# Performance work log

Measured on AMD Instinct MI355X. Metric: run time of the kernel, lower is better.

## Reference

```python
import jax, jax.numpy as jnp
import numpy as np


def _psf2otf(psf, shape):
    """Pad psf to `shape`, circularly shift so kernel center is at (0,0), FFT2."""
    pad = np.zeros(shape, dtype=np.float64)
    pad[: psf.shape[0], : psf.shape[1]] = psf
    for ax, k in enumerate(psf.shape):
        pad = np.roll(pad, -(k // 2), axis=ax)
    return np.fft.fft2(pad)


def setup_inputs() -> dict:
    key = jax.random.key(0)
    B, C, H, W = 32, 3, 512, 512
    output = jax.random.normal(key, (B, C, H, W), dtype=jnp.float32)
    return {"output": output}


def reference(output) -> jnp.ndarray:
    B, C, H, W = output.shape
    # Frequency-domain gradient filters (static, computed at trace time).
    fx = jnp.asarray(_psf2otf(np.array([[-1.0, 1.0]]), (H, W)), dtype=jnp.complex64)
    fy = jnp.asarray(_psf2otf(np.array([[-1.0], [1.0]]), (H, W)), dtype=jnp.complex64)
    # One batched FFT over (B, C, H, W) instead of B*C separate fft2 calls.
    F = jnp.fft.fft2(output)            # (B, C, H, W) complex64
    gx = jnp.fft.ifft2(F * fx)          # horizontal gradient (complex)
    gy = jnp.fft.ifft2(F * fy)          # vertical gradient (complex)
    # torch.norm over the stacked (gx, gy) dim of complex values = sqrt(|gx|^2 + |gy|^2)
    mag = jnp.sqrt(jnp.abs(gx) ** 2 + jnp.abs(gy) ** 2)
    denom = jnp.asarray(B * C * H * W, dtype=mag.dtype)
    return jnp.sum(mag) / denom
```

## Files before the change

### kernel.cpp

```cpp
#include <hip/hip_runtime.h>


#define DIM_H 512
#define DIM_W 512
#define PLANES 96
#define TOTAL (PLANES * DIM_H * DIM_W)
#define NV (TOTAL / 4)
#define NBLOCKS 2048
#define NTHREADS 256

__global__ __launch_bounds__(NTHREADS) void tv_partial(const float* __restrict__ in,
                                                       float* __restrict__ partial) {
    const float4* __restrict__ in4 = (const float4*)in;
    int tid = blockIdx.x * NTHREADS + threadIdx.x;
    float s = 0.0f;

    for (int i = tid; i < NV; i += NBLOCKS * NTHREADS) {
        int p  = i >> 16;
        int r  = i & 65535;
        int y  = r >> 7;
        int x4 = r & 127;

        float4 c = in4[i];

        int ydn = (y + 1) & (DIM_H - 1);
        float4 d = in4[(p << 16) | (ydn << 7) | x4];

        int xw = ((x4 << 2) + 4) & (DIM_W - 1);
        float e = in[(p << 18) + (y << 9) + xw];

        float dx0 = c.x - c.y, dy0 = c.x - d.x;
        float dx1 = c.y - c.z, dy1 = c.y - d.y;
        float dx2 = c.z - c.w, dy2 = c.z - d.z;
        float dx3 = c.w - e,   dy3 = c.w - d.w;

        s += sqrtf(dx0 * dx0 + dy0 * dy0);
        s += sqrtf(dx1 * dx1 + dy1 * dy1);
        s += sqrtf(dx2 * dx2 + dy2 * dy2);
        s += sqrtf(dx3 * dx3 + dy3 * dy3);
    }

    #pragma unroll
    for (int off = 32; off > 0; off >>= 1)
        s += __shfl_down(s, off, 64);

    __shared__ float smem[NTHREADS / 64];
    int lane = threadIdx.x & 63;
    int wave = threadIdx.x >> 6;
    if (lane == 0) smem[wave] = s;
    __syncthreads();
    if (threadIdx.x == 0)
        partial[blockIdx.x] = smem[0] + smem[1] + smem[2] + smem[3];
}

__global__ __launch_bounds__(256) void tv_final(const float* __restrict__ partial,
                                                float* __restrict__ out) {
    float s = 0.0f;
    for (int i = threadIdx.x; i < NBLOCKS; i += 256)
        s += partial[i];

    #pragma unroll
    for (int off = 32; off > 0; off >>= 1)
        s += __shfl_down(s, off, 64);

    __shared__ float smem[4];
    int lane = threadIdx.x & 63;
    int wave = threadIdx.x >> 6;
    if (lane == 0) smem[wave] = s;
    __syncthreads();
    if (threadIdx.x == 0)
        out[0] = (smem[0] + smem[1] + smem[2] + smem[3]) * (1.0f / (float)TOTAL);
}

extern "C" void kernel_launch(void* const* d_in, const int* in_sizes, int n_in,
                              void* d_out, int out_size, void* d_ws, size_t ws_size,
                              hipStream_t stream) {
    const float* in = (const float*)d_in[0];
    float* out = (float*)d_out;
    float* partial = (float*)d_ws;

    tv_partial<<<NBLOCKS, NTHREADS, 0, stream>>>(in, partial);
    tv_final<<<1, 256, 0, stream>>>(partial, out);
}
```

Before: 144.8 us.

## Walk columns down row chunks reusing loaded rows and shuffle right neighbors

Each thread now processes a 16-row vertical strip of one float4 column. The row below is carried forward as the next iteration's centre, so each row is loaded about once instead of twice. The right-neighbour scalar comes from a wave shuffle rather than a separate global load, and only lane 63 does a scalar load. The grid becomes fixed-size (96*32*128/256 blocks) instead of grid-stride, which adds one extra halo row load per chunk.

```diff
diff --git a/kernel.cpp b/kernel.cpp
--- a/kernel.cpp
+++ b/kernel.cpp
@@ -5,39 +5,53 @@
 #define DIM_W 512
 #define PLANES 96
 #define TOTAL (PLANES * DIM_H * DIM_W)
-#define NV (TOTAL / 4)
-#define NBLOCKS 2048
+#define W4 128
+#define CHUNK 16
+#define CHUNKS (DIM_H / CHUNK)
 #define NTHREADS 256
+#define NBLOCKS (PLANES * CHUNKS * W4 / NTHREADS)
 
 __global__ __launch_bounds__(NTHREADS) void tv_partial(const float* __restrict__ in,
                                                        float* __restrict__ partial) {
     const float4* __restrict__ in4 = (const float4*)in;
-    int tid = blockIdx.x * NTHREADS + threadIdx.x;
+    int t = blockIdx.x * NTHREADS + threadIdx.x;
+    int x4    = t & (W4 - 1);
+    int chunk = (t >> 7) & (CHUNKS - 1);
+    int p     = t >> 12;
+
+    int lane = threadIdx.x & 63;
+    int base = (p << 16) + (chunk << 11) + x4;
+    int wrap0 = (p << 16) + x4;
+    int srow = (p << 18) + (((x4 << 2) + 4) & (DIM_W - 1));
+
     float s = 0.0f;
+    int idx = base;
+    float4 c = in4[idx];
 
-    for (int i = tid; i < NV; i += NBLOCKS * NTHREADS) {
-        int p  = i >> 16;
-        int r  = i & 65535;
-        int y  = r >> 7;
-        int x4 = r & 127;
+    #pragma unroll
+    for (int j = 0; j < CHUNK; ++j) {
+        int nidx = idx + W4;
+        if (chunk == CHUNKS - 1 && j == CHUNK - 1) nidx = wrap0;
+        float4 d = in4[nidx];
 
-        float4 c = in4[i];
-
-        int ydn = (y + 1) & (DIM_H - 1);
-        float4 d = in4[(p << 16) | (ydn << 7) | x4];
-
-        int xw = ((x4 << 2) + 4) & (DIM_W - 1);
-        float e = in[(p << 18) + (y << 9) + xw];
+        float ex = __shfl_down(c.x, 1, 64);
+        if (lane == 63) {
+            int y = (chunk << 4) + j;
+            ex = in[srow + (y << 9)];
+        }
 
         float dx0 = c.x - c.y, dy0 = c.x - d.x;
         float dx1 = c.y - c.z, dy1 = c.y - d.y;
         float dx2 = c.z - c.w, dy2 = c.z - d.z;
-        float dx3 = c.w - e,   dy3 = c.w - d.w;
+        float dx3 = c.w - ex,  dy3 = c.w - d.w;
 
         s += sqrtf(dx0 * dx0 + dy0 * dy0);
         s += sqrtf(dx1 * dx1 + dy1 * dy1);
         s += sqrtf(dx2 * dx2 + dy2 * dy2);
         s += sqrtf(dx3 * dx3 + dy3 * dy3);
+
+        c = d;
+        idx += W4;
     }
 
     #pragma unroll
@@ -45,7 +59,6 @@
         s += __shfl_down(s, off, 64);
 
     __shared__ float smem[NTHREADS / 64];
-    int lane = threadIdx.x & 63;
     int wave = threadIdx.x >> 6;
     if (lane == 0) smem[wave] = s;
     __syncthreads();
```

After: 153.9 us. +6.3%, slower.

## Assign each wave a row chunk and reuse the row below across iterations

Applied to the files above, without the earlier changes.

Each wavefront now owns an 8-row strip of one plane, with each lane handling 8 contiguous floats per row. The loaded row below is carried forward as the next iteration's current row, so each row is read once instead of twice. The right-neighbor element comes from a lane shuffle instead of a separate scalar global load. NBLOCKS becomes 1536, so there are fewer threads and each does more work, which lowers latency hiding and parallelism.

```diff
diff --git a/kernel.cpp b/kernel.cpp
--- a/kernel.cpp
+++ b/kernel.cpp
@@ -5,39 +5,58 @@
 #define DIM_W 512
 #define PLANES 96
 #define TOTAL (PLANES * DIM_H * DIM_W)
-#define NV (TOTAL / 4)
-#define NBLOCKS 2048
+#define W4 128
+#define CHUNK 8
+#define CHUNKS (DIM_H / CHUNK)
 #define NTHREADS 256
+#define NBLOCKS (PLANES * CHUNKS / 4)
 
 __global__ __launch_bounds__(NTHREADS) void tv_partial(const float* __restrict__ in,
                                                        float* __restrict__ partial) {
     const float4* __restrict__ in4 = (const float4*)in;
-    int tid = blockIdx.x * NTHREADS + threadIdx.x;
+    int wid  = blockIdx.x * (NTHREADS / 64) + (threadIdx.x >> 6);
+    int lane = threadIdx.x & 63;
+    int p     = wid >> 6;
+    int chunk = wid & (CHUNKS - 1);
+
+    int idx  = (p << 16) + (chunk << 10) + (lane << 1);
+    int wrap = (p << 16) + (lane << 1);
+    int src  = (lane + 1) & 63;
+
+    float4 c0 = in4[idx];
+    float4 c1 = in4[idx + 1];
     float s = 0.0f;
 
-    for (int i = tid; i < NV; i += NBLOCKS * NTHREADS) {
-        int p  = i >> 16;
-        int r  = i & 65535;
-        int y  = r >> 7;
-        int x4 = r & 127;
+    #pragma unroll
+    for (int j = 0; j < CHUNK; ++j) {
+        int nidx = idx + W4;
+        if (chunk == CHUNKS - 1 && j == CHUNK - 1) nidx = wrap;
+        float4 d0 = in4[nidx];
+        float4 d1 = in4[nidx + 1];
 
-        float4 c = in4[i];
+        float e = __shfl(c0.x, src, 64);
 
-        int ydn = (y + 1) & (DIM_H - 1);
-        float4 d = in4[(p << 16) | (ydn << 7) | x4];
-
-        int xw = ((x4 << 2) + 4) & (DIM_W - 1);
-        float e = in[(p << 18) + (y << 9) + xw];
-
-        float dx0 = c.x - c.y, dy0 = c.x - d.x;
-        float dx1 = c.y - c.z, dy1 = c.y - d.y;
-        float dx2 = c.z - c.w, dy2 = c.z - d.z;
-        float dx3 = c.w - e,   dy3 = c.w - d.w;
+        float dx0 = c0.x - c0.y, dy0 = c0.x - d0.x;
+        float dx1 = c0.y - c0.z, dy1 = c0.y - d0.y;
+        float dx2 = c0.z - c0.w, dy2 = c0.z - d0.z;
+        float dx3 = c0.w - c1.x, dy3 = c0.w - d0.w;
+        float dx4 = c1.x - c1.y, dy4 = c1.x - d1.x;
+        float dx5 = c1.y - c1.z, dy5 = c1.y - d1.y;
+        float dx6 = c1.z - c1.w, dy6 = c1.z - d1.z;
+        float dx7 = c1.w - e,    dy7 = c1.w - d1.w;
 
         s += sqrtf(dx0 * dx0 + dy0 * dy0);
         s += sqrtf(dx1 * dx1 + dy1 * dy1);
         s += sqrtf(dx2 * dx2 + dy2 * dy2);
         s += sqrtf(dx3 * dx3 + dy3 * dy3);
+        s += sqrtf(dx4 * dx4 + dy4 * dy4);
+        s += sqrtf(dx5 * dx5 + dy5 * dy5);
+        s += sqrtf(dx6 * dx6 + dy6 * dy6);
+        s += sqrtf(dx7 * dx7 + dy7 * dy7);
+
+        c0 = d0;
+        c1 = d1;
+        idx = nidx;
     }
 
     #pragma unroll
@@ -45,7 +64,6 @@
         s += __shfl_down(s, off, 64);
 
     __shared__ float smem[NTHREADS / 64];
-    int lane = threadIdx.x & 63;
     int wave = threadIdx.x >> 6;
     if (lane == 0) smem[wave] = s;
     __syncthreads();
```

Result: no change. 147.4 us (+1.7%).

## Assign each wave a 4-row strip and share neighbors via shuffles

Applied to the files above, without the earlier changes.

Replaces the grid-stride loop with one 4-row strip per wavefront. Each wave loads 5 rows as float4 registers, reuses the row below across iterations, and gets the right-hand neighbor through cross-lane shuffles instead of a separate scalar load. This reduces redundant global loads, since each row is read about 1.25 times instead of 2 plus a scalar, and it removes loop index arithmetic. In exchange the grid grows to 3072 blocks with no looping, and each wave has less memory-level parallelism.

```diff
diff --git a/kernel.cpp b/kernel.cpp
--- a/kernel.cpp
+++ b/kernel.cpp
@@ -5,47 +5,61 @@
 #define DIM_W 512
 #define PLANES 96
 #define TOTAL (PLANES * DIM_H * DIM_W)
-#define NV (TOTAL / 4)
-#define NBLOCKS 2048
+#define W4 128
+#define STRIPS_PER_PLANE 128
 #define NTHREADS 256
+#define NBLOCKS (PLANES * STRIPS_PER_PLANE / 4)
 
 __global__ __launch_bounds__(NTHREADS) void tv_partial(const float* __restrict__ in,
                                                        float* __restrict__ partial) {
     const float4* __restrict__ in4 = (const float4*)in;
-    int tid = blockIdx.x * NTHREADS + threadIdx.x;
+    int wid  = blockIdx.x * (NTHREADS / 64) + (threadIdx.x >> 6);
+    int lane = threadIdx.x & 63;
+    int p = wid >> 7;
+    int k = wid & (STRIPS_PER_PLANE - 1);
+
+    int rb  = (p << 16) + (k << 9) + lane;
+    int rb4 = (k == STRIPS_PER_PLANE - 1) ? ((p << 16) + lane)
+                                          : (rb + 4 * W4);
+
+    float4 a0 = in4[rb];            float4 b0 = in4[rb + 64];
+    float4 a1 = in4[rb + 128];      float4 b1 = in4[rb + 192];
+    float4 a2 = in4[rb + 256];      float4 b2 = in4[rb + 320];
+    float4 a3 = in4[rb + 384];      float4 b3 = in4[rb + 448];
+    float4 a4 = in4[rb4];           float4 b4 = in4[rb4 + 64];
+
+    int src = (lane + 1) & 63;
+    bool last = (lane == 63);
     float s = 0.0f;
 
-    for (int i = tid; i < NV; i += NBLOCKS * NTHREADS) {
-        int p  = i >> 16;
-        int r  = i & 65535;
-        int y  = r >> 7;
-        int x4 = r & 127;
+#define TV_ROW(A, B, DA, DB)                                                   \
+    do {                                                                       \
+        float n0 = __shfl((A).x, src, 64);                                     \
+        float n1 = __shfl((B).x, src, 64);                                     \
+        float e0 = last ? n1 : n0;              \
+        float e1 = last ? n0 : n1;          \
+        float t;                                                               \
+        t = (A).x - (A).y; s += sqrtf(t*t + ((A).x-(DA).x)*((A).x-(DA).x));    \
+        t = (A).y - (A).z; s += sqrtf(t*t + ((A).y-(DA).y)*((A).y-(DA).y));    \
+        t = (A).z - (A).w; s += sqrtf(t*t + ((A).z-(DA).z)*((A).z-(DA).z));    \
+        t = (A).w - e0;    s += sqrtf(t*t + ((A).w-(DA).w)*((A).w-(DA).w));    \
+        t = (B).x - (B).y; s += sqrtf(t*t + ((B).x-(DB).x)*((B).x-(DB).x));    \
+        t = (B).y - (B).z; s += sqrtf(t*t + ((B).y-(DB).y)*((B).y-(DB).y));    \
+        t = (B).z - (B).w; s += sqrtf(t*t + ((B).z-(DB).z)*((B).z-(DB).z));    \
+        t = (B).w - e1;    s += sqrtf(t*t + ((B).w-(DB).w)*((B).w-(DB).w));    \
+    } while (0)
 
-        float4 c = in4[i];
-
-        int ydn = (y + 1) & (DIM_H - 1);
-        float4 d = in4[(p << 16) | (ydn << 7) | x4];
-
-        int xw = ((x4 << 2) + 4) & (DIM_W - 1);
-        float e = in[(p << 18) + (y << 9) + xw];
-
-        float dx0 = c.x - c.y, dy0 = c.x - d.x;
-        float dx1 = c.y - c.z, dy1 = c.y - d.y;
-        float dx2 = c.z - c.w, dy2 = c.z - d.z;
-        float dx3 = c.w - e,   dy3 = c.w - d.w;
-
-        s += sqrtf(dx0 * dx0 + dy0 * dy0);
-        s += sqrtf(dx1 * dx1 + dy1 * dy1);
-        s += sqrtf(dx2 * dx2 + dy2 * dy2);
-        s += sqrtf(dx3 * dx3 + dy3 * dy3);
-    }
+    TV_ROW(a0, b0, a1, b1);
+    TV_ROW(a1, b1, a2, b2);
+    TV_ROW(a2, b2, a3, b3);
+    TV_ROW(a3, b3, a4, b4);
+#undef TV_ROW
 
     #pragma unroll
     for (int off = 32; off > 0; off >>= 1)
         s += __shfl_down(s, off, 64);
 
     __shared__ float smem[NTHREADS / 64];
-    int lane = threadIdx.x & 63;
     int wave = threadIdx.x >> 6;
     if (lane == 0) smem[wave] = s;
     __syncthreads();
```

Measured after the change: 145.8 us. Within noise of the previous version (+0.7%).
